# Kernel tuning notes

Measured on AMD Instinct MI355X. Metric: run time of the kernel, lower is better.

## Reference

```python
import jax, jax.numpy as jnp
import numpy as np

N_EMBD = 1024
HEAD_SIZE = 64
BLOCK_SIZE = 512
BATCH = 4


def setup_inputs() -> dict:
    key = jax.random.key(0)
    ks = jax.random.split(key, 5)
    T = BLOCK_SIZE
    x = jax.random.normal(ks[0], (BATCH, 2 * T - 1, N_EMBD), dtype=jnp.float32)
    scale = 1.0 / np.sqrt(N_EMBD)
    Wk = jax.random.normal(ks[1], (N_EMBD, HEAD_SIZE), dtype=jnp.float32) * scale
    Wv = jax.random.normal(ks[2], (N_EMBD, HEAD_SIZE), dtype=jnp.float32) * scale
    Wq = jax.random.normal(ks[3], (N_EMBD, HEAD_SIZE), dtype=jnp.float32) * scale
    # keyWindowBias in torch has shape (1,1,head_size,block_size); store as (hs, T)
    bias = jax.random.normal(ks[4], (HEAD_SIZE, T), dtype=jnp.float32)
    return {"x": x, "Wk": Wk, "Wv": Wv, "Wq": Wq, "bias": bias}


def reference(x, Wk, Wv, Wq, bias):
    B, S, C = x.shape
    T = (S + 1) // 2  # S == 2*T - 1 (block_size)
    xToPred = x[:, -T:, :]
    # block_layer == 0 path: project full sequence for k, v
    k = jnp.einsum('bsc,cd->bsd', x, Wk)        # [B, 2T-1, hs]
    v = jnp.einsum('bsc,cd->bsd', x, Wv)        # [B, 2T-1, hs]
    q = jnp.einsum('btc,cd->btd', xToPred, Wq)  # [B, T, hs]

    # sliding windows: window w covers positions w..w+T-1 (torch unfold semantics)
    idx = jnp.arange(T)[:, None] + jnp.arange(T)[None, :]  # [T, T]

    k_win = k[:, idx, :] + bias.T[None, None, :, :]  # [B, T, T, hs] + [1,1,T,hs]
    wei = jnp.einsum('bwd,bwtd->bwt', q, k_win)      # [B, T, T]
    wei = jax.nn.softmax(wei, axis=-1)

    v_win = v[:, idx, :]                              # [B, T, T, hs]
    out = jnp.einsum('bwt,bwtd->bwd', wei, v_win)     # [B, T, hs]
    return out
```

## Files before the change

### kernel.cpp

```cpp
#include <hip/hip_runtime.h>
#include <hip/hip_bf16.h>

#define BB 4
#define SS 1023
#define TT 512
#define CC 1024
#define DD 64
#define NROW (BB*SS)
#define NROWP 4096

typedef float f4 __attribute__((ext_vector_type(4)));
typedef float f2 __attribute__((ext_vector_type(2)));
typedef short bf16x8 __attribute__((ext_vector_type(8)));
typedef short s4 __attribute__((ext_vector_type(4)));
typedef float f32x4 __attribute__((ext_vector_type(4)));

__device__ __forceinline__ unsigned split_rtn(float v) {
    const unsigned u  = __builtin_bit_cast(unsigned, v);
    const unsigned r  = u + 0x7FFFu + ((u >> 16) & 1u);
    const unsigned hi = r >> 16;
    const float hif   = __builtin_bit_cast(float, r & 0xFFFF0000u);
    const float res   = v - hif;
    const unsigned u2 = __builtin_bit_cast(unsigned, res);
    const unsigned r2 = u2 + 0x7FFFu + ((u2 >> 16) & 1u);
    return (r2 & 0xFFFF0000u) | hi;
}

__global__ __launch_bounds__(64) void wsplit_kernel(
    const float* __restrict__ Wk,
    const float* __restrict__ Wv,
    const float* __restrict__ Wq,
    unsigned short* __restrict__ bwh,
    unsigned short* __restrict__ bwl)
{
    const int f    = blockIdx.x;
    const int p    = f >> 7;
    const int rem  = f & 127;
    const int nsub = rem >> 5;
    const int ks   = rem & 31;
    const int lane = threadIdx.x;
    const int quad = lane >> 4, l4 = lane & 15;
    const float* W = (p == 0) ? Wk : (p == 1) ? Wv : Wq;
    const int n = nsub * 16 + l4;

    bf16x8 h, l;
#pragma unroll
    for (int j = 0; j < 8; ++j) {
        const int k = ks * 32 + quad * 8 + j;
        const unsigned hl = split_rtn(W[k * DD + n]);
        h[j] = (short)(hl & 0xFFFFu);
        l[j] = (short)(hl >> 16);
    }
    ((bf16x8*)bwh)[f * 64 + lane] = h;
    ((bf16x8*)bwl)[f * 64 + lane] = l;
}

__global__ __launch_bounds__(256) void proj_fused_kernel(
    const float* __restrict__ x,
    const unsigned short* __restrict__ bwh,
    const unsigned short* __restrict__ bwl,
    float* __restrict__ kT,
    float* __restrict__ vbuf,
    float* __restrict__ qbuf)
{
    __shared__ __align__(16) unsigned short lh[16 * 1024];
    __shared__ __align__(16) unsigned short ll[16 * 1024];

    const int blk  = blockIdx.x;
    const int p    = blk % 3;
    const int mt   = blk / 3;
    const int bs0  = mt * 16;
    const int tid  = threadIdx.x;

    {
        const int k = tid * 4;
#pragma unroll 4
        for (int i = 0; i < 16; ++i) {
            int arow = bs0 + i; if (arow > NROW - 1) arow = NROW - 1;
            const f4 xv = *(const f4*)(x + (size_t)arow * CC + k);
            s4 h, l;
#pragma unroll
            for (int j = 0; j < 4; ++j) {
                const unsigned hl = split_rtn(xv[j]);
                h[j] = (short)(hl & 0xFFFFu);
                l[j] = (short)(hl >> 16);
            }
            const int idx = i * 1024 + (k ^ ((i & 7) << 3));
            *(s4*)&lh[idx] = h;
            *(s4*)&ll[idx] = l;
        }
    }
    __syncthreads();

    const int lane = tid & 63;
    const int w    = tid >> 6;
    const int quad = lane >> 4, l4 = lane & 15;

    const bf16x8* bh = (const bf16x8*)bwh
                     + (size_t)((p * 4 + w) * 32) * 64 + lane;
    const bf16x8* bl = (const bf16x8*)bwl
                     + (size_t)((p * 4 + w) * 32) * 64 + lane;

    const int rbase = l4 * 1024;
    const int kxor  = (l4 & 7) << 3;

    f32x4 acc = {0.f, 0.f, 0.f, 0.f};
#pragma unroll 4
    for (int ks = 0; ks < 32; ++ks) {
        const int k0 = ks * 32 + quad * 8;
        const bf16x8 ah = *(const bf16x8*)&lh[rbase + (k0 ^ kxor)];
        const bf16x8 al = *(const bf16x8*)&ll[rbase + (k0 ^ kxor)];
        const bf16x8 bhn = bh[ks * 64];
        const bf16x8 bln = bl[ks * 64];
        acc = __builtin_amdgcn_mfma_f32_16x16x32_bf16(ah, bhn, acc, 0, 0, 0);
        acc = __builtin_amdgcn_mfma_f32_16x16x32_bf16(ah, bln, acc, 0, 0, 0);
        acc = __builtin_amdgcn_mfma_f32_16x16x32_bf16(al, bhn, acc, 0, 0, 0);
        acc = __builtin_amdgcn_mfma_f32_16x16x32_bf16(al, bln, acc, 0, 0, 0);
    }

    {
        const int d = w * 16 + l4;
#pragma unroll
        for (int reg = 0; reg < 4; ++reg) {
            const int bs = bs0 + quad * 4 + reg;
            if (bs < NROW) {
                const float val = acc[reg];
                const int b = bs / SS, ss = bs - b * SS;
                if (p == 0) {
                    kT[(size_t)d * NROWP + b * 1024 + ss] = val;
                } else if (p == 1) {
                    vbuf[(size_t)bs * DD + d] = val;
                } else {
                    if (ss >= TT - 1)
                        qbuf[((size_t)b * TT + (ss - (TT - 1))) * DD + d] = val;
                }
            }
        }
    }
}

__global__ __launch_bounds__(512) void attn_kernel(
    const float* __restrict__ kT,
    const float* __restrict__ vbuf,
    const float* __restrict__ qbuf,
    const float* __restrict__ bias,
    float* __restrict__ out)
{
    __shared__ __align__(16) float qsT[DD][8];
    __shared__ __align__(8) float part[2][8][TT];
    __shared__ float weiT[TT][9];
    __shared__ float invs[8];
    __shared__ float partial[8][8][DD];

    const int tid  = threadIdx.x;
    const int lane = tid & 63;
    const int wv   = tid >> 6;
    const int blk  = blockIdx.x;
    const int b    = blk >> 6;
    const int w0   = (blk & 63) * 8;

    if (tid < 8 * DD) {
        const int m = tid >> 6, dd = tid & 63;
        qsT[dd][m] = qbuf[((size_t)b * TT + w0 + m) * DD + dd];
    }
    __syncthreads();

    {
        const int h = tid >> 8, p = tid & 255;
        const int t0 = 2 * p;
        const float* kcol = kT + (size_t)(32 * h) * NROWP + b * 1024 + w0 + t0;
        const float* bp   = bias + (size_t)(32 * h) * TT + t0;
        float am[8][2];
#pragma unroll
        for (int m = 0; m < 8; ++m) { am[m][0] = 0.f; am[m][1] = 0.f; }
#pragma unroll 4
        for (int i = 0; i < 32; ++i) {
            const float* kr = kcol + (size_t)i * NROWP;
            const f2 k01 = *(const f2*)kr;
            const f2 k23 = *(const f2*)(kr + 2);
            const f2 k45 = *(const f2*)(kr + 4);
            const f2 k67 = *(const f2*)(kr + 6);
            const float k8 = kr[8];
            const f2 bv = *(const f2*)(bp + (size_t)i * TT);
            const f4 qA = *(const f4*)&qsT[32 * h + i][0];
            const f4 qB = *(const f4*)&qsT[32 * h + i][4];
            const float kk[9] = {k01[0], k01[1], k23[0], k23[1],
                                 k45[0], k45[1], k67[0], k67[1], k8};
            const float qq[8] = {qA[0], qA[1], qA[2], qA[3],
                                 qB[0], qB[1], qB[2], qB[3]};
#pragma unroll
            for (int m = 0; m < 8; ++m) {
                am[m][0] = fmaf(qq[m], kk[m],     am[m][0]);
                am[m][0] = fmaf(qq[m], bv[0],     am[m][0]);
                am[m][1] = fmaf(qq[m], kk[m + 1], am[m][1]);
                am[m][1] = fmaf(qq[m], bv[1],     am[m][1]);
            }
        }
#pragma unroll
        for (int m = 0; m < 8; ++m)
            *(f2*)&part[h][m][t0] = (f2){am[m][0], am[m][1]};
    }
    __syncthreads();

    {
        const int m = wv;
        float r[8];
#pragma unroll
        for (int j = 0; j < 8; ++j) {
            const int t = lane + 64 * j;
            r[j] = part[0][m][t] + part[1][m][t];
        }
        float mx = r[0];
#pragma unroll
        for (int j = 1; j < 8; ++j) mx = fmaxf(mx, r[j]);
#pragma unroll
        for (int off = 1; off < 64; off <<= 1)
            mx = fmaxf(mx, __shfl_xor(mx, off, 64));
        float sum = 0.f;
#pragma unroll
        for (int j = 0; j < 8; ++j) {
            const float e = __expf(r[j] - mx);
            weiT[lane + 64 * j][m] = e;
            sum += e;
        }
#pragma unroll
        for (int off = 1; off < 64; off <<= 1)
            sum += __shfl_xor(sum, off, 64);
        if (lane == 0) invs[m] = 1.f / sum;
    }
    __syncthreads();

    {
        const int t0r = wv * 64;
        const float* vb = vbuf + ((size_t)b * SS + w0 + t0r) * DD + lane;
        float pm[8];
#pragma unroll
        for (int m = 0; m < 8; ++m) pm[m] = 0.f;
        float vv[8];
#pragma unroll
        for (int m = 0; m < 7; ++m) vv[m] = vb[(size_t)m * DD];
#pragma unroll 2
        for (int t = 0; t < 64; ++t) {
            vv[7] = vb[(size_t)(t + 7) * DD];
            const float* wt = &weiT[t0r + t][0];
#pragma unroll
            for (int m = 0; m < 8; ++m)
                pm[m] = fmaf(wt[m], vv[m], pm[m]);
#pragma unroll
            for (int m = 0; m < 7; ++m) vv[m] = vv[m + 1];
        }
#pragma unroll
        for (int m = 0; m < 8; ++m)
            partial[wv][m][lane] = pm[m];
    }
    __syncthreads();

    {
        const int m = tid >> 6, dd = tid & 63;
        float o = 0.f;
#pragma unroll
        for (int j = 0; j < 8; ++j) o += partial[j][m][dd];
        out[((size_t)b * TT + w0 + m) * DD + dd] = o * invs[m];
    }
}

extern "C" void kernel_launch(void* const* d_in, const int* in_sizes, int n_in,
                              void* d_out, int out_size, void* d_ws, size_t ws_size,
                              hipStream_t stream) {
    const float* x    = (const float*)d_in[0];
    const float* Wk   = (const float*)d_in[1];
    const float* Wv   = (const float*)d_in[2];
    const float* Wq   = (const float*)d_in[3];
    const float* bias = (const float*)d_in[4];
    float* out = (float*)d_out;

    char* ws = (char*)d_ws;
    float* kT             = (float*)(ws + 0);
    float* vbuf           = (float*)(ws + (2u  << 20));
    float* qbuf           = (float*)(ws + (4u  << 20));
    unsigned short* bwh   = (unsigned short*)(ws + (6u  << 20));
    unsigned short* bwl   = (unsigned short*)(ws + (8u  << 20));

    wsplit_kernel<<<384, 64, 0, stream>>>(Wk, Wv, Wq, bwh, bwl);
    proj_fused_kernel<<<768, 256, 0, stream>>>(x, bwh, bwl, kT, vbuf, qbuf);
    attn_kernel<<<BB * TT / 8, 512, 0, stream>>>(kT, vbuf, qbuf, bias, out);
}
```

Before: 107.4 us.

## Merge weight split, projection and attention into one cooperative persistent kernel

```diff
diff --git a/kernel.cpp b/kernel.cpp
--- a/kernel.cpp
+++ b/kernel.cpp
@@ -1,5 +1,8 @@
 #include <hip/hip_runtime.h>
 #include <hip/hip_bf16.h>
+#include <hip/hip_cooperative_groups.h>
+
+namespace cg = cooperative_groups;
 
 #define BB 4
 #define SS 1023
@@ -26,241 +29,253 @@
     return (r2 & 0xFFFF0000u) | hi;
 }
 
-__global__ __launch_bounds__(64) void wsplit_kernel(
+__global__ __launch_bounds__(512, 1) void mega_kernel(
+    const float* __restrict__ x,
     const float* __restrict__ Wk,
     const float* __restrict__ Wv,
     const float* __restrict__ Wq,
-    unsigned short* __restrict__ bwh,
-    unsigned short* __restrict__ bwl)
-{
-    const int f    = blockIdx.x;
-    const int p    = f >> 7;
-    const int rem  = f & 127;
-    const int nsub = rem >> 5;
-    const int ks   = rem & 31;
-    const int lane = threadIdx.x;
-    const int quad = lane >> 4, l4 = lane & 15;
-    const float* W = (p == 0) ? Wk : (p == 1) ? Wv : Wq;
-    const int n = nsub * 16 + l4;
-
-    bf16x8 h, l;
-#pragma unroll
-    for (int j = 0; j < 8; ++j) {
-        const int k = ks * 32 + quad * 8 + j;
-        const unsigned hl = split_rtn(W[k * DD + n]);
-        h[j] = (short)(hl & 0xFFFFu);
-        l[j] = (short)(hl >> 16);
-    }
-    ((bf16x8*)bwh)[f * 64 + lane] = h;
-    ((bf16x8*)bwl)[f * 64 + lane] = l;
-}
-
-__global__ __launch_bounds__(256) void proj_fused_kernel(
-    const float* __restrict__ x,
-    const unsigned short* __restrict__ bwh,
-    const unsigned short* __restrict__ bwl,
+    const float* __restrict__ bias,
     float* __restrict__ kT,
     float* __restrict__ vbuf,
-    float* __restrict__ qbuf)
-{
-    __shared__ __align__(16) unsigned short lh[16 * 1024];
-    __shared__ __align__(16) unsigned short ll[16 * 1024];
-
-    const int blk  = blockIdx.x;
-    const int p    = blk % 3;
-    const int mt   = blk / 3;
-    const int bs0  = mt * 16;
-    const int tid  = threadIdx.x;
-
-    {
-        const int k = tid * 4;
-#pragma unroll 4
-        for (int i = 0; i < 16; ++i) {
-            int arow = bs0 + i; if (arow > NROW - 1) arow = NROW - 1;
-            const f4 xv = *(const f4*)(x + (size_t)arow * CC + k);
-            s4 h, l;
-#pragma unroll
-            for (int j = 0; j < 4; ++j) {
-                const unsigned hl = split_rtn(xv[j]);
-                h[j] = (short)(hl & 0xFFFFu);
-                l[j] = (short)(hl >> 16);
-            }
-            const int idx = i * 1024 + (k ^ ((i & 7) << 3));
-            *(s4*)&lh[idx] = h;
-            *(s4*)&ll[idx] = l;
-        }
-    }
-    __syncthreads();
-
-    const int lane = tid & 63;
-    const int w    = tid >> 6;
-    const int quad = lane >> 4, l4 = lane & 15;
-
-    const bf16x8* bh = (const bf16x8*)bwh
-                     + (size_t)((p * 4 + w) * 32) * 64 + lane;
-    const bf16x8* bl = (const bf16x8*)bwl
-                     + (size_t)((p * 4 + w) * 32) * 64 + lane;
-
-    const int rbase = l4 * 1024;
-    const int kxor  = (l4 & 7) << 3;
-
-    f32x4 acc = {0.f, 0.f, 0.f, 0.f};
-#pragma unroll 4
-    for (int ks = 0; ks < 32; ++ks) {
-        const int k0 = ks * 32 + quad * 8;
-        const bf16x8 ah = *(const bf16x8*)&lh[rbase + (k0 ^ kxor)];
-        const bf16x8 al = *(const bf16x8*)&ll[rbase + (k0 ^ kxor)];
-        const bf16x8 bhn = bh[ks * 64];
-        const bf16x8 bln = bl[ks * 64];
-        acc = __builtin_amdgcn_mfma_f32_16x16x32_bf16(ah, bhn, acc, 0, 0, 0);
-        acc = __builtin_amdgcn_mfma_f32_16x16x32_bf16(ah, bln, acc, 0, 0, 0);
-        acc = __builtin_amdgcn_mfma_f32_16x16x32_bf16(al, bhn, acc, 0, 0, 0);
-        acc = __builtin_amdgcn_mfma_f32_16x16x32_bf16(al, bln, acc, 0, 0, 0);
-    }
-
-    {
-        const int d = w * 16 + l4;
-#pragma unroll
-        for (int reg = 0; reg < 4; ++reg) {
-            const int bs = bs0 + quad * 4 + reg;
-            if (bs < NROW) {
-                const float val = acc[reg];
-                const int b = bs / SS, ss = bs - b * SS;
-                if (p == 0) {
-                    kT[(size_t)d * NROWP + b * 1024 + ss] = val;
-                } else if (p == 1) {
-                    vbuf[(size_t)bs * DD + d] = val;
-                } else {
-                    if (ss >= TT - 1)
-                        qbuf[((size_t)b * TT + (ss - (TT - 1))) * DD + d] = val;
-                }
-            }
-        }
-    }
-}
-
-__global__ __launch_bounds__(512) void attn_kernel(
-    const float* __restrict__ kT,
-    const float* __restrict__ vbuf,
-    const float* __restrict__ qbuf,
-    const float* __restrict__ bias,
+    float* __restrict__ qbuf,
+    unsigned short* __restrict__ bwh,
+    unsigned short* __restrict__ bwl,
     float* __restrict__ out)
 {
-    __shared__ __align__(16) float qsT[DD][8];
-    __shared__ __align__(8) float part[2][8][TT];
-    __shared__ float weiT[TT][9];
-    __shared__ float invs[8];
-    __shared__ float partial[8][8][DD];
+    __shared__ __align__(16) union SMem {
+        struct {
+            unsigned short lh[2][16 * 1024];
+            unsigned short ll[2][16 * 1024];
+        } p;
+        struct {
+            float qsT[DD][8];
+            float part[2][8][TT];
+            float weiT[TT][9];
+            float invs[8];
+            float partial[8][8][DD];
+        } a;
+    } sm;
 
     const int tid  = threadIdx.x;
     const int lane = tid & 63;
     const int wv   = tid >> 6;
-    const int blk  = blockIdx.x;
-    const int b    = blk >> 6;
-    const int w0   = (blk & 63) * 8;
-
-    if (tid < 8 * DD) {
-        const int m = tid >> 6, dd = tid & 63;
-        qsT[dd][m] = qbuf[((size_t)b * TT + w0 + m) * DD + dd];
+    cg::grid_group grid = cg::this_grid();
+
+    {
+        const int gw = blockIdx.x * 8 + wv;
+        if (gw < 384) {
+            const int f    = gw;
+            const int p    = f >> 7;
+            const int rem  = f & 127;
+            const int nsub = rem >> 5;
+            const int ks   = rem & 31;
+            const int quad = lane >> 4, l4 = lane & 15;
+            const float* W = (p == 0) ? Wk : (p == 1) ? Wv : Wq;
+            const int n = nsub * 16 + l4;
+
+            bf16x8 h, l;
+#pragma unroll
+            for (int j = 0; j < 8; ++j) {
+                const int k = ks * 32 + quad * 8 + j;
+                const unsigned hl = split_rtn(W[k * DD + n]);
+                h[j] = (short)(hl & 0xFFFFu);
+                l[j] = (short)(hl >> 16);
+            }
+            ((bf16x8*)bwh)[f * 64 + lane] = h;
+            ((bf16x8*)bwl)[f * 64 + lane] = l;
+        }
     }
-    __syncthreads();
+    __threadfence();
+    grid.sync();
+
+    for (int su = blockIdx.x; su < 384; su += 256) {
+        const int half = wv >> 2;
+        const int unit = su * 2 + half;
+        const int p    = unit % 3;
+        const int mt   = unit / 3;
+        const int bs0  = mt * 16;
+        const int ltid = tid & 255;
+        unsigned short* lh = sm.p.lh[half];
+        unsigned short* ll = sm.p.ll[half];
+
+        {
+            const int k = ltid * 4;
+#pragma unroll 4
+            for (int i = 0; i < 16; ++i) {
+                int arow = bs0 + i; if (arow > NROW - 1) arow = NROW - 1;
+                const f4 xv = *(const f4*)(x + (size_t)arow * CC + k);
+                s4 h, l;
+#pragma unroll
+                for (int j = 0; j < 4; ++j) {
+                    const unsigned hl = split_rtn(xv[j]);
+                    h[j] = (short)(hl & 0xFFFFu);
+                    l[j] = (short)(hl >> 16);
+                }
+                const int idx = i * 1024 + (k ^ ((i & 7) << 3));
+                *(s4*)&lh[idx] = h;
+                *(s4*)&ll[idx] = l;
+            }
+        }
+        __syncthreads();
+
+        {
+            const int llane = ltid & 63;
+            const int w     = ltid >> 6;
+            const int quad  = llane >> 4, l4 = llane & 15;
+
+            const bf16x8* bh = (const bf16x8*)bwh
+                             + (size_t)((p * 4 + w) * 32) * 64 + llane;
+            const bf16x8* bl = (const bf16x8*)bwl
+                             + (size_t)((p * 4 + w) * 32) * 64 + llane;
+
+            const int rbase = l4 * 1024;
+            const int kxor  = (l4 & 7) << 3;
+
+            f32x4 acc = {0.f, 0.f, 0.f, 0.f};
+#pragma unroll 4
+            for (int ks = 0; ks < 32; ++ks) {
+                const int k0 = ks * 32 + quad * 8;
+                const bf16x8 ah = *(const bf16x8*)&lh[rbase + (k0 ^ kxor)];
+                const bf16x8 al = *(const bf16x8*)&ll[rbase + (k0 ^ kxor)];
+                const bf16x8 bhn = bh[ks * 64];
+                const bf16x8 bln = bl[ks * 64];
+                acc = __builtin_amdgcn_mfma_f32_16x16x32_bf16(ah, bhn, acc, 0, 0, 0);
+                acc = __builtin_amdgcn_mfma_f32_16x16x32_bf16(ah, bln, acc, 0, 0, 0);
+                acc = __builtin_amdgcn_mfma_f32_16x16x32_bf16(al, bhn, acc, 0, 0, 0);
+                acc = __builtin_amdgcn_mfma_f32_16x16x32_bf16(al, bln, acc, 0, 0, 0);
+            }
+
+            const int d = w * 16 + l4;
+#pragma unroll
+            for (int reg = 0; reg < 4; ++reg) {
+                const int bs = bs0 + quad * 4 + reg;
+                if (bs < NROW) {
+                    const float val = acc[reg];
+                    const int b = bs / SS, ss = bs - b * SS;
+                    if (p == 0) {
+                        kT[(size_t)d * NROWP + b * 1024 + ss] = val;
+                    } else if (p == 1) {
+                        vbuf[(size_t)bs * DD + d] = val;
+                    } else {
+                        if (ss >= TT - 1)
+                            qbuf[((size_t)b * TT + (ss - (TT - 1))) * DD + d] = val;
+                    }
+                }
+            }
+        }
+        __syncthreads();
+    }
+    __threadfence();
+    grid.sync();
 
     {
-        const int h = tid >> 8, p = tid & 255;
-        const int t0 = 2 * p;
-        const float* kcol = kT + (size_t)(32 * h) * NROWP + b * 1024 + w0 + t0;
-        const float* bp   = bias + (size_t)(32 * h) * TT + t0;
-        float am[8][2];
-#pragma unroll
-        for (int m = 0; m < 8; ++m) { am[m][0] = 0.f; am[m][1] = 0.f; }
+        const int blk = blockIdx.x;
+        const int b   = blk >> 6;
+        const int w0  = (blk & 63) * 8;
+
+        {
+            const int m = tid >> 6, dd = tid & 63;
+            sm.a.qsT[dd][m] = qbuf[((size_t)b * TT + w0 + m) * DD + dd];
+        }
+        __syncthreads();
+
+        {
+            const int h = tid >> 8, p = tid & 255;
+            const int t0 = 2 * p;
+            const float* kcol = kT + (size_t)(32 * h) * NROWP + b * 1024 + w0 + t0;
+            const float* bp   = bias + (size_t)(32 * h) * TT + t0;
+            float am[8][2];
+#pragma unroll
+            for (int m = 0; m < 8; ++m) { am[m][0] = 0.f; am[m][1] = 0.f; }
 #pragma unroll 4
-        for (int i = 0; i < 32; ++i) {
-            const float* kr = kcol + (size_t)i * NROWP;
-            const f2 k01 = *(const f2*)kr;
-            const f2 k23 = *(const f2*)(kr + 2);
-            const f2 k45 = *(const f2*)(kr + 4);
-            const f2 k67 = *(const f2*)(kr + 6);
-            const float k8 = kr[8];
-            const f2 bv = *(const f2*)(bp + (size_t)i * TT);
-            const f4 qA = *(const f4*)&qsT[32 * h + i][0];
-            const f4 qB = *(const f4*)&qsT[32 * h + i][4];
-            const float kk[9] = {k01[0], k01[1], k23[0], k23[1],
-                                 k45[0], k45[1], k67[0], k67[1], k8};
-            const float qq[8] = {qA[0], qA[1], qA[2], qA[3],
-                                 qB[0], qB[1], qB[2], qB[3]};
-#pragma unroll
-            for (int m = 0; m < 8; ++m) {
-                am[m][0] = fmaf(qq[m], kk[m],     am[m][0]);
-                am[m][0] = fmaf(qq[m], bv[0],     am[m][0]);
-                am[m][1] = fmaf(qq[m], kk[m + 1], am[m][1]);
-                am[m][1] = fmaf(qq[m], bv[1],     am[m][1]);
-            }
-        }
-#pragma unroll
-        for (int m = 0; m < 8; ++m)
-            *(f2*)&part[h][m][t0] = (f2){am[m][0], am[m][1]};
-    }
-    __syncthreads();
-
-    {
-        const int m = wv;
-        float r[8];
-#pragma unroll
-        for (int j = 0; j < 8; ++j) {
-            const int t = lane + 64 * j;
-            r[j] = part[0][m][t] + part[1][m][t];
-        }
-        float mx = r[0];
-#pragma unroll
-        for (int j = 1; j < 8; ++j) mx = fmaxf(mx, r[j]);
-#pragma unroll
-        for (int off = 1; off < 64; off <<= 1)
-            mx = fmaxf(mx, __shfl_xor(mx, off, 64));
-        float sum = 0.f;
-#pragma unroll
-        for (int j = 0; j < 8; ++j) {
-            const float e = __expf(r[j] - mx);
-            weiT[lane + 64 * j][m] = e;
-            sum += e;
-        }
-#pragma unroll
-        for (int off = 1; off < 64; off <<= 1)
-            sum += __shfl_xor(sum, off, 64);
-        if (lane == 0) invs[m] = 1.f / sum;
-    }
-    __syncthreads();
-
-    {
-        const int t0r = wv * 64;
-        const float* vb = vbuf + ((size_t)b * SS + w0 + t0r) * DD + lane;
-        float pm[8];
-#pragma unroll
-        for (int m = 0; m < 8; ++m) pm[m] = 0.f;
-        float vv[8];
-#pragma unroll
-        for (int m = 0; m < 7; ++m) vv[m] = vb[(size_t)m * DD];
+            for (int i = 0; i < 32; ++i) {
+                const float* kr = kcol + (size_t)i * NROWP;
+                const f2 k01 = *(const f2*)kr;
+                const f2 k23 = *(const f2*)(kr + 2);
+                const f2 k45 = *(const f2*)(kr + 4);
+                const f2 k67 = *(const f2*)(kr + 6);
+                const float k8 = kr[8];
+                const f2 bv = *(const f2*)(bp + (size_t)i * TT);
+                const f4 qA = *(const f4*)&sm.a.qsT[32 * h + i][0];
+                const f4 qB = *(const f4*)&sm.a.qsT[32 * h + i][4];
+                const float kk[9] = {k01[0], k01[1], k23[0], k23[1],
+                                     k45[0], k45[1], k67[0], k67[1], k8};
+                const float qq[8] = {qA[0], qA[1], qA[2], qA[3],
+                                     qB[0], qB[1], qB[2], qB[3]};
+#pragma unroll
+                for (int m = 0; m < 8; ++m) {
+                    am[m][0] = fmaf(qq[m], kk[m],     am[m][0]);
+                    am[m][0] = fmaf(qq[m], bv[0],     am[m][0]);
+                    am[m][1] = fmaf(qq[m], kk[m + 1], am[m][1]);
+                    am[m][1] = fmaf(qq[m], bv[1],     am[m][1]);
+                }
+            }
+#pragma unroll
+            for (int m = 0; m < 8; ++m)
+                *(f2*)&sm.a.part[h][m][t0] = (f2){am[m][0], am[m][1]};
+        }
+        __syncthreads();
+
+        {
+            const int m = wv;
+            float r[8];
+#pragma unroll
+            for (int j = 0; j < 8; ++j) {
+                const int t = lane + 64 * j;
+                r[j] = sm.a.part[0][m][t] + sm.a.part[1][m][t];
+            }
+            float mx = r[0];
+#pragma unroll
+            for (int j = 1; j < 8; ++j) mx = fmaxf(mx, r[j]);
+#pragma unroll
+            for (int off = 1; off < 64; off <<= 1)
+                mx = fmaxf(mx, __shfl_xor(mx, off, 64));
+            float sum = 0.f;
+#pragma unroll
+            for (int j = 0; j < 8; ++j) {
+                const float e = __expf(r[j] - mx);
+                sm.a.weiT[lane + 64 * j][m] = e;
+                sum += e;
+            }
+#pragma unroll
+            for (int off = 1; off < 64; off <<= 1)
+                sum += __shfl_xor(sum, off, 64);
+            if (lane == 0) sm.a.invs[m] = 1.f / sum;
+        }
+        __syncthreads();
+
+        {
+            const int t0r = wv * 64;
+            const float* vb = vbuf + ((size_t)b * SS + w0 + t0r) * DD + lane;
+            float pm[8];
+#pragma unroll
+            for (int m = 0; m < 8; ++m) pm[m] = 0.f;
+            float vvv[8];
+#pragma unroll
+            for (int m = 0; m < 7; ++m) vvv[m] = vb[(size_t)m * DD];
 #pragma unroll 2
-        for (int t = 0; t < 64; ++t) {
-            vv[7] = vb[(size_t)(t + 7) * DD];
-            const float* wt = &weiT[t0r + t][0];
+            for (int t = 0; t < 64; ++t) {
+                vvv[7] = vb[(size_t)(t + 7) * DD];
+                const float* wt = &sm.a.weiT[t0r + t][0];
+#pragma unroll
+                for (int m = 0; m < 8; ++m)
+                    pm[m] = fmaf(wt[m], vvv[m], pm[m]);
+#pragma unroll
+                for (int m = 0; m < 7; ++m) vvv[m] = vvv[m + 1];
+            }
 #pragma unroll
             for (int m = 0; m < 8; ++m)
-                pm[m] = fmaf(wt[m], vv[m], pm[m]);
-#pragma unroll
-            for (int m = 0; m < 7; ++m) vv[m] = vv[m + 1];
-        }
-#pragma unroll
-        for (int m = 0; m < 8; ++m)
-            partial[wv][m][lane] = pm[m];
-    }
-    __syncthreads();
-
-    {
-        const int m = tid >> 6, dd = tid & 63;
-        float o = 0.f;
-#pragma unroll
-        for (int j = 0; j < 8; ++j) o += partial[j][m][dd];
-        out[((size_t)b * TT + w0 + m) * DD + dd] = o * invs[m];
+                sm.a.partial[wv][m][lane] = pm[m];
+        }
+        __syncthreads();
+
+        {
+            const int m = tid >> 6, dd = tid & 63;
+            float o = 0.f;
+#pragma unroll
+            for (int j = 0; j < 8; ++j) o += sm.a.partial[j][m][dd];
+            out[((size_t)b * TT + w0 + m) * DD + dd] = o * sm.a.invs[m];
+        }
     }
 }
 
@@ -281,7 +296,11 @@
     unsigned short* bwh   = (unsigned short*)(ws + (6u  << 20));
     unsigned short* bwl   = (unsigned short*)(ws + (8u  << 20));
 
-    wsplit_kernel<<<384, 64, 0, stream>>>(Wk, Wv, Wq, bwh, bwl);
-    proj_fused_kernel<<<768, 256, 0, stream>>>(x, bwh, bwl, kT, vbuf, qbuf);
-    attn_kernel<<<BB * TT / 8, 512, 0, stream>>>(kT, vbuf, qbuf, bias, out);
+    void* args[] = {
+        (void*)&x, (void*)&Wk, (void*)&Wv, (void*)&Wq, (void*)&bias,
+        (void*)&kT, (void*)&vbuf, (void*)&qbuf, (void*)&bwh, (void*)&bwl,
+        (void*)&out
+    };
+    hipLaunchCooperativeKernel((const void*)mega_kernel,
+                               dim3(256), dim3(512), args, 0, stream);
 }
```

After: 259.2 us. 2.41x slower.
